# Kernel tuning notes

Hardware: AMD Instinct MI355X
Metric: run time of the kernel (lower is better)

The kernel has to match this reference:

```python
import jax, jax.numpy as jnp
import numpy as np

# dims
B, E, D1, D2 = 16, 384, 64, 64
WS1, WS2 = 8, 8                 # window sizes
H = 12                          # heads
HID = 1536                      # mlp hidden
NW = (D1 // WS1) * (D2 // WS2)  # 64 windows
S = WS1 * WS2                   # 64 tokens per window
DH = E // H                     # 32 head dim


def _layernorm(x, g, b, eps=1e-5):
    mu = jnp.mean(x, axis=-1, keepdims=True)
    var = jnp.var(x, axis=-1, keepdims=True)
    return (x - mu) * jax.lax.rsqrt(var + eps) * g + b


def setup_inputs() -> dict:
    key = jax.random.key(0)
    ks = jax.random.split(key, 10)
    sc = 0.02
    return {
        "x": jax.random.normal(ks[0], (B, E, D1, D2), jnp.float32),
        "mask": jax.random.normal(ks[1], (1, NW, 1, S, S), jnp.float32),
        "ln1_g": jnp.ones((E,), jnp.float32),
        "ln1_b": jnp.zeros((E,), jnp.float32),
        "Wq": sc * jax.random.normal(ks[2], (E, E), jnp.float32),
        "bq": jnp.zeros((E,), jnp.float32),
        "Wk": sc * jax.random.normal(ks[3], (E, E), jnp.float32),
        "bk": jnp.zeros((E,), jnp.float32),
        "Wv": sc * jax.random.normal(ks[4], (E, E), jnp.float32),
        "bv": jnp.zeros((E,), jnp.float32),
        "Wo": sc * jax.random.normal(ks[5], (E, E), jnp.float32),
        "bo": jnp.zeros((E,), jnp.float32),
        "pos_bias": sc * jax.random.normal(ks[6], (1, 1, H, S, S), jnp.float32),
        "ln2_g": jnp.ones((E,), jnp.float32),
        "ln2_b": jnp.zeros((E,), jnp.float32),
        "Wm1": sc * jax.random.normal(ks[7], (E, HID), jnp.float32),
        "bm1": jnp.zeros((HID,), jnp.float32),
        "Wm2": sc * jax.random.normal(ks[8], (HID, E), jnp.float32),
        "bm2": jnp.zeros((E,), jnp.float32),
    }


def reference(x, mask, ln1_g, ln1_b, Wq, bq, Wk, bk, Wv, bv, Wo, bo,
              pos_bias, ln2_g, ln2_b, Wm1, bm1, Wm2, bm2):
    scale = DH ** -0.5
    # channels-last: (b, d1, d2, e)
    xt = jnp.transpose(x, (0, 2, 3, 1))
    xn = _layernorm(xt, ln1_g, ln1_b)
    # cyclic shift (shifted window)
    xn = jnp.roll(xn, (-WS1 // 2, -WS2 // 2), axis=(1, 2))
    # window partition -> (b, nw, s, e)
    xw = xn.reshape(B, D1 // WS1, WS1, D2 // WS2, WS2, E)
    xw = xw.transpose(0, 1, 3, 2, 4, 5).reshape(B, NW, S, E)
    # qkv
    q = (xw @ Wq + bq) * scale
    k = xw @ Wk + bk
    v = xw @ Wv + bv
    q = q.reshape(B, NW, S, H, DH).transpose(0, 1, 3, 2, 4)  # b,w,h,s,d
    k = k.reshape(B, NW, S, H, DH).transpose(0, 1, 3, 2, 4)
    v = v.reshape(B, NW, S, H, DH).transpose(0, 1, 3, 2, 4)
    attn = jnp.einsum('bwhsd,bwhtd->bwhst', q, k) + pos_bias + mask
    attn = jax.nn.softmax(attn, axis=-1)
    z = jnp.einsum('bwhst,bwhtd->bwhsd', attn, v)
    z = z.transpose(0, 1, 3, 2, 4).reshape(B, NW, S, E)
    z = z @ Wo + bo
    # window reverse -> (b, d1, d2, e)
    z = z.reshape(B, D1 // WS1, D2 // WS2, WS1, WS2, E)
    z = z.transpose(0, 1, 3, 2, 4, 5).reshape(B, D1, D2, E)
    z = jnp.roll(z, (WS1 // 2, WS2 // 2), axis=(1, 2))
    xt = xt + z
    # MLP (note: GELU after BOTH linears, faithful to source)
    y = _layernorm(xt, ln2_g, ln2_b)
    y = jax.nn.gelu(y @ Wm1 + bm1, approximate=False)
    y = jax.nn.gelu(y @ Wm2 + bm2, approximate=False)
    xt = xt + y
    # back to channels-first (b, e, d1, d2)
    return jnp.transpose(xt, (0, 3, 1, 2))
```

## Files before the change

kernel.cpp:

```cpp
#include <hip/hip_runtime.h>
#include <hip/hip_bf16.h>
#include <math.h>

#define B_    16
#define E_    384
#define P_    4096
#define NW_   64
#define S_    64
#define H_    12
#define DH_   32
#define HID_  1536
#define T_    65536
#define SHIFT_ 4

typedef unsigned short ushort_t;
typedef __attribute__((ext_vector_type(8))) __bf16 b8;
typedef __attribute__((ext_vector_type(8))) ushort_t u8v;
typedef __attribute__((ext_vector_type(4))) float f4;
typedef __attribute__((ext_vector_type(4))) unsigned u32x4;

__device__ __forceinline__ float u2f(ushort_t u){
    return __uint_as_float(((unsigned)u) << 16);
}
__device__ __forceinline__ ushort_t f2u(float f){
    union { __hip_bfloat16 h; ushort_t u; } cv;
    cv.h = __float2bfloat16(f);
    return cv.u;
}
__device__ __forceinline__ unsigned pack2(float lo, float hi){
    return (unsigned)f2u(lo) | ((unsigned)f2u(hi) << 16);
}
__device__ __forceinline__ float gelu_f(float v){
    const float y2 = v * (1.5957691216057308f + 0.0713548162726f * v * v);
    return v * __builtin_amdgcn_rcpf(1.f + __expf(-y2));
}

#define MFMA(a,b,c) __builtin_amdgcn_mfma_f32_16x16x32_bf16((a),(b),(c),0,0,0)

#define GL2LDS(gp, lp) \
    __builtin_amdgcn_global_load_lds((const __attribute__((address_space(1))) void*)(gp), \
                                     (__attribute__((address_space(3))) void*)(lp), 16, 0, 0)

template<int PERM>
__device__ __forceinline__ int rowmap(int m){
    if (PERM == 0) return m;
    const int bl = m >> 12, wn = (m >> 6) & 63, sd = m & 63;
    const int i_ = ((wn >> 3) << 3) + (sd >> 3);
    const int j_ = ((wn & 7) << 3) + (sd & 7);
    const int d1 = (i_ + SHIFT_) & 63;
    const int d2 = (j_ + SHIFT_) & 63;
    return (bl << 12) + (d1 << 6) + d2;
}

__device__ void wt_body(int bx, int by, int tid,
    const float* __restrict__ src, ushort_t* __restrict__ dst, int K, int N,
    float scale, const float* __restrict__ gv)
{
    __shared__ float t[32][33];
    const int k0 = bx * 32, n0 = by * 32;
    const int c = tid & 31, r = tid >> 5;
    for (int rr = r; rr < 32; rr += 8)
        t[rr][c] = src[(size_t)(k0 + rr) * N + n0 + c];
    __syncthreads();
    const float gg = (gv ? gv[k0 + c] : 1.f) * scale;
    for (int rr = r; rr < 32; rr += 8)
        dst[(size_t)(n0 + rr) * K + k0 + c] = f2u(t[c][rr] * gg);
}

__device__ void lnfold_body(int bx, int tid,
    const float* __restrict__ W, const float* __restrict__ g,
    const float* __restrict__ bt, float scale, int N,
    float* __restrict__ S1, float* __restrict__ S2)
{
    __shared__ float r1[8][32], r2[8][32];
    const int c = tid & 31, ks = tid >> 5;
    const int n = bx * 32 + c;
    float s1 = 0.f, s2 = 0.f;
#pragma unroll
    for (int i = 0; i < 48; ++i){
        const int k = ks * 48 + i;
        const float w = W[(size_t)k * N + n];
        s1 += g[k] * w;
        s2 += bt[k] * w;
    }
    r1[ks][c] = s1; r2[ks][c] = s2;
    __syncthreads();
    if (tid < 32){
        float a = 0.f, b2 = 0.f;
#pragma unroll
        for (int j = 0; j < 8; ++j){ a += r1[j][tid]; b2 += r2[j][tid]; }
        S1[bx * 32 + tid] = a * scale;
        S2[bx * 32 + tid] = b2 * scale;
    }
}

__global__ __launch_bounds__(256) void prep_all(
    const float* Wq, const float* Wk, const float* Wv, const float* Wo,
    const float* Wm1, const float* Wm2,
    const float* ln1_g, const float* ln1_b,
    const float* ln2_g, const float* ln2_b,
    const float* bq, const float* bk, const float* bv,
    ushort_t* Wqkvt, ushort_t* Wot, ushort_t* Wm1t, ushort_t* Wm2t,
    float* S1q, float* S2q, float* S1m, float* S2m, float* bqkv)
{
    const float qscale = 0.17677669529663687f;
    const int id = blockIdx.x, tid = threadIdx.x;
    if (id < 144)       wt_body(id % 12, id / 12, tid, Wq, Wqkvt, E_, E_, qscale, ln1_g);
    else if (id < 288){ const int l = id - 144; wt_body(l % 12, l / 12, tid, Wk, Wqkvt + 384 * E_, E_, E_, 1.f, ln1_g); }
    else if (id < 432){ const int l = id - 288; wt_body(l % 12, l / 12, tid, Wv, Wqkvt + 768 * E_, E_, E_, 1.f, ln1_g); }
    else if (id < 576){ const int l = id - 432; wt_body(l % 12, l / 12, tid, Wo, Wot, E_, E_, 1.f, nullptr); }
    else if (id < 1152){ const int l = id - 576; wt_body(l % 12, l / 12, tid, Wm1, Wm1t, E_, HID_, 1.f, ln2_g); }
    else if (id < 1728){ const int l = id - 1152; wt_body(l % 48, l / 48, tid, Wm2, Wm2t, HID_, E_, 1.f, nullptr); }
    else if (id < 1740) lnfold_body(id - 1728, tid, Wq, ln1_g, ln1_b, qscale, E_, S1q, S2q);
    else if (id < 1752) lnfold_body(id - 1740, tid, Wk, ln1_g, ln1_b, 1.f, E_, S1q + 384, S2q + 384);
    else if (id < 1764) lnfold_body(id - 1752, tid, Wv, ln1_g, ln1_b, 1.f, E_, S1q + 768, S2q + 768);
    else if (id < 1812) lnfold_body(id - 1764, tid, Wm1, ln2_g, ln2_b, 1.f, HID_, S1m, S2m);
    else {
        const int i = (id - 1812) * 256 + tid;
        if (i < 1152){
            float v;
            if (i < 384)      v = bq[i] * qscale;
            else if (i < 768) v = bk[i - 384];
            else              v = bv[i - 768];
            bqkv[i] = v;
        }
    }
}

__global__ __launch_bounds__(256) void k1_ln_window(
    const float* __restrict__ x, ushort_t* __restrict__ xt,
    float* __restrict__ mu1w, float* __restrict__ rs1w)
{
    __shared__ ushort_t tile[64][E_ + 2];
    __shared__ float redS[4][64], redQ[4][64];
    const int b = blockIdx.y, p0 = blockIdx.x * 64, tid = threadIdx.x;

    {
        const int pq = tid & 15, e00 = tid >> 4;
        const float* xp = x + ((size_t)b * E_ + e00) * P_ + p0 + pq * 4;
        f4 v[24];
#pragma unroll
        for (int i = 0; i < 24; ++i)
            v[i] = *(const f4*)(xp + (size_t)(i * 16) * P_);
        float s0 = 0.f, s1 = 0.f, s2 = 0.f, s3 = 0.f;
        float q0 = 0.f, q1 = 0.f, q2 = 0.f, q3 = 0.f;
#pragma unroll
        for (int i = 0; i < 24; ++i){
            const int e = e00 + i * 16;
            tile[pq * 4 + 0][e] = f2u(v[i][0]);
            tile[pq * 4 + 1][e] = f2u(v[i][1]);
            tile[pq * 4 + 2][e] = f2u(v[i][2]);
            tile[pq * 4 + 3][e] = f2u(v[i][3]);
            s0 += v[i][0]; q0 += v[i][0] * v[i][0];
            s1 += v[i][1]; q1 += v[i][1] * v[i][1];
            s2 += v[i][2]; q2 += v[i][2] * v[i][2];
            s3 += v[i][3]; q3 += v[i][3] * v[i][3];
        }
        s0 += __shfl_xor(s0, 16); q0 += __shfl_xor(q0, 16);
        s1 += __shfl_xor(s1, 16); q1 += __shfl_xor(q1, 16);
        s2 += __shfl_xor(s2, 16); q2 += __shfl_xor(q2, 16);
        s3 += __shfl_xor(s3, 16); q3 += __shfl_xor(q3, 16);
        s0 += __shfl_xor(s0, 32); q0 += __shfl_xor(q0, 32);
        s1 += __shfl_xor(s1, 32); q1 += __shfl_xor(q1, 32);
        s2 += __shfl_xor(s2, 32); q2 += __shfl_xor(q2, 32);
        s3 += __shfl_xor(s3, 32); q3 += __shfl_xor(q3, 32);
        const int lane = tid & 63, wvi = tid >> 6;
        if (lane < 16){
            redS[wvi][pq * 4 + 0] = s0; redQ[wvi][pq * 4 + 0] = q0;
            redS[wvi][pq * 4 + 1] = s1; redQ[wvi][pq * 4 + 1] = q1;
            redS[wvi][pq * 4 + 2] = s2; redQ[wvi][pq * 4 + 2] = q2;
            redS[wvi][pq * 4 + 3] = s3; redQ[wvi][pq * 4 + 3] = q3;
        }
    }
    __syncthreads();
    if (tid < 64){
        const float s  = redS[0][tid] + redS[1][tid] + redS[2][tid] + redS[3][tid];
        const float ss = redQ[0][tid] + redQ[1][tid] + redQ[2][tid] + redQ[3][tid];
        const float mu = s / E_;
        const float rs = rsqrtf(ss / E_ - mu * mu + 1e-5f);
        const int p = p0 + tid;
        const int d1 = p >> 6, d2 = p & 63;
        const int i_ = (d1 + 64 - SHIFT_) & 63;
        const int j_ = (d2 + 64 - SHIFT_) & 63;
        const int wsd = ((((i_ >> 3) << 3) + (j_ >> 3)) << 6)
                      + ((i_ & 7) << 3) + (j_ & 7);
        mu1w[b * P_ + wsd] = mu;
        rs1w[b * P_ + wsd] = rs;
    }

    unsigned* xtu = (unsigned*)xt;
    for (int it = 0; it < 48; ++it){
        const int idx = it * 256 + tid;
        const int pj = idx / 192, ep = idx - pj * 192;
        xtu[((size_t)b * P_ + p0 + pj) * 192 + ep] = *(const unsigned*)&tile[pj][ep * 2];
    }
}

template<int KST, int AS, int OS, int MODE, int LNF, int PERM>
__global__ __launch_bounds__(256, 3) void gemm128(
    const ushort_t* __restrict__ A, const ushort_t* __restrict__ Bm,
    const float* __restrict__ bias, ushort_t* __restrict__ out,
    const float* __restrict__ mu, const float* __restrict__ rs,
    const float* __restrict__ S1, const float* __restrict__ S2,
    const ushort_t* __restrict__ resid)
{
    __shared__ __align__(16) ushort_t lds[24576];
    const int tid = threadIdx.x, lane = tid & 63, wv = tid >> 6;
    const int l15 = lane & 15, l4 = lane >> 4;
    const int wr = wv >> 1, wc = wv & 1;

    const int gx = gridDim.x;
    const int nwg = gx * gridDim.y;
    const int d = blockIdx.y * gx + blockIdx.x;
    const int cpx = nwg >> 3;
    const int lb = (d & 7) * cpx + (d >> 3);
    const int n0 = (lb % gx) * 128;
    const size_t m0 = (size_t)(lb / gx) * 128;

    const int kq = tid & 3;
    const int xq = kq ^ ((tid >> 3) & 3);
    size_t aoff0, aoff1, boff0, boff1;
    {
        const int r0 = (int)m0 + (tid >> 2);
        aoff0 = (size_t)rowmap<PERM>(r0) * AS + xq * 8;
        aoff1 = (size_t)rowmap<PERM>(r0 + 64) * AS + xq * 8;
        const int nr = n0 + (tid >> 2);
        boff0 = (size_t)nr * (KST * 32) + xq * 8;
        boff1 = boff0 + (size_t)64 * (KST * 32);
    }

#define STG(cur, k0) do { \
        ushort_t* dst_ = lds + (cur) * 8192; \
        GL2LDS(A + aoff0 + (k0), dst_ + tid * 8); \
        GL2LDS(A + aoff1 + (k0), dst_ + (256 + tid) * 8); \
        GL2LDS(Bm + boff0 + (k0), dst_ + 4096 + tid * 8); \
        GL2LDS(Bm + boff1 + (k0), dst_ + 4096 + (256 + tid) * 8); \
    } while (0)

    f4 acc[4][4];
#pragma unroll
    for (int i = 0; i < 4; ++i)
#pragma unroll
        for (int j = 0; j < 4; ++j) acc[i][j] = (f4){0.f, 0.f, 0.f, 0.f};

    const int rq = (l4 ^ ((l15 >> 1) & 3)) * 8;

    STG(0, 0);
    STG(1, 32);
    for (int ks = 0; ks < KST; ++ks){
        if (ks < KST - 1) asm volatile("s_waitcnt vmcnt(4)" ::: "memory");
        else              asm volatile("s_waitcnt vmcnt(0)" ::: "memory");
        __builtin_amdgcn_s_barrier();
        asm volatile("" ::: "memory");
        if (ks + 2 < KST) STG((ks + 2) % 3, (ks + 2) * 32);
        asm volatile("" ::: "memory");
        const ushort_t* Al = lds + (ks % 3) * 8192;
        const ushort_t* Bl = Al + 4096;
        b8 ax[4], aw[4];
#pragma unroll
        for (int f = 0; f < 4; ++f){
            ax[f] = *(const b8*)(Al + (wr * 64 + f * 16 + l15) * 32 + rq);
            aw[f] = *(const b8*)(Bl + (wc * 64 + f * 16 + l15) * 32 + rq);
        }
        __builtin_amdgcn_s_setprio(1);
#pragma unroll
        for (int fm = 0; fm < 4; ++fm)
#pragma unroll
            for (int fn = 0; fn < 4; ++fn)
                acc[fm][fn] = MFMA(aw[fn], ax[fm], acc[fm][fn]);
        __builtin_amdgcn_s_setprio(0);
    }
#undef STG

    if (MODE == 4){
        float* Tf = (float*)lds;
        float* outf = (float*)out;
#pragma unroll
        for (int rg = 0; rg < 4; ++rg){
            __syncthreads();
            if (wr == (rg >> 1)){
#pragma unroll
                for (int f2h = 0; f2h < 2; ++f2h){
                    const int fm = (rg & 1) * 2 + f2h;
                    const int m5 = f2h * 16 + l15;
                    const int grow = (int)m0 + rg * 32 + m5;
#pragma unroll
                    for (int fn = 0; fn < 4; ++fn){
                        const f4 v = acc[fm][fn];
                        const int nc = wc * 64 + fn * 16 + l4 * 4;
                        const f4 bb = *(const f4*)(bias + n0 + nc);
                        const uint2 ov = *(const uint2*)(resid + (size_t)grow * E_ + n0 + nc);
                        Tf[(nc + 0) * 36 + m5] = u2f((ushort_t)ov.x)         + gelu_f(v[0] + bb[0]);
                        Tf[(nc + 1) * 36 + m5] = u2f((ushort_t)(ov.x >> 16)) + gelu_f(v[1] + bb[1]);
                        Tf[(nc + 2) * 36 + m5] = u2f((ushort_t)ov.y)         + gelu_f(v[2] + bb[2]);
                        Tf[(nc + 3) * 36 + m5] = u2f((ushort_t)(ov.y >> 16)) + gelu_f(v[3] + bb[3]);
                    }
                }
            }
            __syncthreads();
            {
                const int growb = (int)m0 + rg * 32;
                const int bl = growb >> 12, p12 = growb & 4095;
                const int po = (tid & 3) * 4;
#pragma unroll
                for (int eh = 0; eh < 2; ++eh){
                    const int e = eh * 64 + (tid >> 2);
                    float* op = outf + ((size_t)bl * E_ + n0 + e) * P_ + p12 + po;
                    const float* tp = &Tf[e * 36 + po];
                    __builtin_nontemporal_store(*(const f4*)tp, (f4*)op);
                    __builtin_nontemporal_store(*(const f4*)(tp + 16), (f4*)(op + 16));
                }
            }
        }
        return;
    }

    ushort_t* bounce = lds + wv * 2304;
    const int l8r = lane >> 3, l8c = lane & 7;
#pragma unroll
    for (int hh = 0; hh < 2; ++hh){
#pragma unroll
        for (int f2 = 0; f2 < 2; ++f2){
            const int fm = hh * 2 + f2;
            float mur = 0.f, rsr = 1.f;
            if (LNF){
                const int gm = (int)m0 + wr * 64 + fm * 16 + l15;
                mur = mu[gm]; rsr = rs[gm];
            }
#pragma unroll
            for (int fn = 0; fn < 4; ++fn){
                const f4 v = acc[fm][fn];
                const int nc = n0 + wc * 64 + fn * 16 + l4 * 4;
                const f4 bb = *(const f4*)(bias + nc);
                f4 w;
                if (LNF){
                    const f4 s1 = *(const f4*)(S1 + nc);
                    const f4 s2 = *(const f4*)(S2 + nc);
#pragma unroll
                    for (int r = 0; r < 4; ++r)
                        w[r] = rsr * v[r] - rsr * mur * s1[r] + s2[r] + bb[r];
                } else {
#pragma unroll
                    for (int r = 0; r < 4; ++r) w[r] = v[r] + bb[r];
                }
                uint2 pk;
                if (MODE == 1 || MODE == 2){
                    pk.x = pack2(gelu_f(w[0]), gelu_f(w[1]));
                    pk.y = pack2(gelu_f(w[2]), gelu_f(w[3]));
                } else {
                    pk.x = pack2(w[0], w[1]);
                    pk.y = pack2(w[2], w[3]);
                }
                *(uint2*)(bounce + (f2 * 16 + l15) * 72 + fn * 16 + l4 * 4) = pk;
            }
        }
#pragma unroll
        for (int i = 0; i < 4; ++i){
            const int br = i * 8 + l8r;
            const int grow = (int)m0 + wr * 64 + hh * 32 + br;
            const b8 yv = *(const b8*)(bounce + br * 72 + l8c * 8);
            size_t orow;
            if (MODE == 3){
                orow = (size_t)rowmap<1>(grow);
            } else {
                orow = (size_t)grow;
            }
            ushort_t* px = out + orow * OS + n0 + wc * 64 + l8c * 8;
            if (MODE >= 2){
                const b8 ov = *(const b8*)px;
                union { b8 v; unsigned u[4]; } o;
#pragma unroll
                for (int j = 0; j < 4; ++j)
                    o.u[j] = pack2((float)ov[2 * j] + (float)yv[2 * j],
                                   (float)ov[2 * j + 1] + (float)yv[2 * j + 1]);
                *(b8*)px = o.v;
            } else if (MODE == 0){
                union { b8 v; u32x4 q; } t; t.v = yv;
                __builtin_nontemporal_store(t.q, (u32x4*)px);
            } else {
                *(b8*)px = yv;
            }
        }
    }
}

__global__ __launch_bounds__(256) void k2b_attn(
    const ushort_t* __restrict__ qkv,
    const float* __restrict__ pb, const float* __restrict__ mk,
    ushort_t* __restrict__ z)
{
    __shared__ __align__(16) ushort_t q_lds[64 * 32];
    __shared__ __align__(16) ushort_t k_lds[64 * 32];
    __shared__ __align__(16) ushort_t vt_lds[32 * 72];
    __shared__ __align__(16) ushort_t P_lds[64 * 72];

    const int w = blockIdx.x, bl = blockIdx.y, hz = blockIdx.z;
    const int tid = threadIdx.x, lane = tid & 63, wv = tid >> 6;
    const int l15 = lane & 15, l4 = lane >> 4;
    const int rowbase = (bl * NW_ + w) * S_;

    const int srow = tid >> 2, sqp = tid & 3;
    const int sfq = sqp ^ ((srow >> 1) & 3);
    const ushort_t* gql = qkv + (size_t)(rowbase + srow) * 1152 + sfq * 8;
    const ushort_t* gvl = qkv + (size_t)(rowbase + srow) * 1152 + 768 + sqp * 8;

    f4 mkr[4];
#pragma unroll
    for (int nt = 0; nt < 4; ++nt){
        const int t = nt * 16 + l15;
#pragma unroll
        for (int r = 0; r < 4; ++r){
            const int sw = wv * 16 + l4 * 4 + r;
            mkr[nt][r] = mk[((size_t)w * S_ + sw) * S_ + t];
        }
    }

    for (int hi = 0; hi < 4; ++hi){
        const int h = hz * 4 + hi;
        const int hb = h * 32;
        GL2LDS(gql + hb, q_lds + tid * 8);
        GL2LDS(gql + 384 + hb, k_lds + tid * 8);
        {
            const u8v vv = *(const u8v*)(gvl + hb);
#pragma unroll
            for (int j = 0; j < 8; ++j)
                vt_lds[(sqp * 8 + j) * 72 + srow] = vv[j];
        }
        __syncthreads();

        {
            const int qr = wv * 16 + l15;
            const int uq = qr * 4 + (l4 ^ ((qr >> 1) & 3));
            const b8 qfrag = *(const b8*)(&q_lds[uq * 8]);
            f4 sacc[4];
#pragma unroll
            for (int nt = 0; nt < 4; ++nt){
                const int kr = nt * 16 + l15;
                const int uk = kr * 4 + (l4 ^ ((kr >> 1) & 3));
                const b8 kfrag = *(const b8*)(&k_lds[uk * 8]);
                f4 c = (f4){0.f, 0.f, 0.f, 0.f};
                c = MFMA(qfrag, kfrag, c);
                const int t = nt * 16 + l15;
#pragma unroll
                for (int r = 0; r < 4; ++r){
                    const int sw = wv * 16 + l4 * 4 + r;
                    c[r] += pb[((size_t)h * S_ + sw) * S_ + t] + mkr[nt][r];
                }
                sacc[nt] = c;
            }
#pragma unroll
            for (int r = 0; r < 4; ++r){
                float m = fmaxf(fmaxf(sacc[0][r], sacc[1][r]),
                                fmaxf(sacc[2][r], sacc[3][r]));
                m = fmaxf(m, __shfl_xor(m, 1));
                m = fmaxf(m, __shfl_xor(m, 2));
                m = fmaxf(m, __shfl_xor(m, 4));
                m = fmaxf(m, __shfl_xor(m, 8));
                const float e0 = __expf(sacc[0][r] - m), e1 = __expf(sacc[1][r] - m);
                const float e2 = __expf(sacc[2][r] - m), e3 = __expf(sacc[3][r] - m);
                float s = e0 + e1 + e2 + e3;
                s += __shfl_xor(s, 1); s += __shfl_xor(s, 2);
                s += __shfl_xor(s, 4); s += __shfl_xor(s, 8);
                const float inv = __builtin_amdgcn_rcpf(s);
                const int row = wv * 16 + l4 * 4 + r;
                P_lds[row * 72 +      l15] = f2u(e0 * inv);
                P_lds[row * 72 + 16 + l15] = f2u(e1 * inv);
                P_lds[row * 72 + 32 + l15] = f2u(e2 * inv);
                P_lds[row * 72 + 48 + l15] = f2u(e3 * inv);
            }
        }

        {
            f4 zacc[2];
#pragma unroll
            for (int nt = 0; nt < 2; ++nt) zacc[nt] = (f4){0.f, 0.f, 0.f, 0.f};
#pragma unroll
            for (int kb = 0; kb < 2; ++kb){
                const b8 pfrag = *(const b8*)(&P_lds[(wv * 16 + l15) * 72 + kb * 32 + l4 * 8]);
#pragma unroll
                for (int nt = 0; nt < 2; ++nt){
                    const b8 vfrag = *(const b8*)(&vt_lds[(nt * 16 + l15) * 72 + kb * 32 + l4 * 8]);
                    zacc[nt] = MFMA(pfrag, vfrag, zacc[nt]);
                }
            }
#pragma unroll
            for (int nt = 0; nt < 2; ++nt)
#pragma unroll
                for (int r = 0; r < 4; ++r){
                    const int row = wv * 16 + l4 * 4 + r;
                    z[(size_t)(rowbase + row) * E_ + hb + nt * 16 + l15] = f2u(zacc[nt][r]);
                }
        }
        __syncthreads();
    }
}

__global__ __launch_bounds__(256) void ln2_stats(
    const ushort_t* __restrict__ xt, float* __restrict__ mu2, float* __restrict__ rs2)
{
    const int tid = threadIdx.x;
    const int lr = blockIdx.x * 64 + (tid >> 2), q = tid & 3;
    const ushort_t* rp = xt + (size_t)lr * E_;
    float s = 0.f, ss = 0.f;
#pragma unroll
    for (int i = 0; i < 12; ++i){
        const b8 v = *(const b8*)(rp + q * 8 + i * 32);
#pragma unroll
        for (int j = 0; j < 8; ++j){ const float f = (float)v[j]; s += f; ss += f * f; }
    }
    s += __shfl_xor(s, 1); ss += __shfl_xor(ss, 1);
    s += __shfl_xor(s, 2); ss += __shfl_xor(ss, 2);
    if (q == 0){
        const float m = s * (1.f / E_);
        mu2[lr] = m;
        rs2[lr] = rsqrtf(ss * (1.f / E_) - m * m + 1e-5f);
    }
}

__global__ __launch_bounds__(256) void k4_out(
    const ushort_t* __restrict__ xt, float* __restrict__ out)
{
    __shared__ float tile[32][68];
    const int b = blockIdx.z, p0 = blockIdx.x * 64, e0 = blockIdx.y * 32;
    const int tid = threadIdx.x;
    {
        const int r = tid >> 2, c = tid & 3;
        const u8v v = *(const u8v*)(xt + ((size_t)b * P_ + p0 + r) * E_ + e0 + c * 8);
#pragma unroll
        for (int j = 0; j < 8; ++j)
            tile[c * 8 + j][r] = u2f(v[j]);
    }
    __syncthreads();
    {
        const int er = tid >> 3, pc = tid & 7;
        float* op = out + ((size_t)b * E_ + e0 + er) * P_ + p0 + pc * 8;
        const f4 v0 = *(const f4*)&tile[er][pc * 8];
        const f4 v1 = *(const f4*)&tile[er][pc * 8 + 4];
        __builtin_nontemporal_store(v0, (f4*)op);
        __builtin_nontemporal_store(v1, (f4*)(op + 4));
    }
}

extern "C" void kernel_launch(void* const* d_in, const int* in_sizes, int n_in,
                              void* d_out, int out_size, void* d_ws, size_t ws_size,
                              hipStream_t stream)
{
    const float* x      = (const float*)d_in[0];
    const float* mask   = (const float*)d_in[1];
    const float* ln1_g  = (const float*)d_in[2];
    const float* ln1_b  = (const float*)d_in[3];
    const float* Wq     = (const float*)d_in[4];
    const float* bq     = (const float*)d_in[5];
    const float* Wk     = (const float*)d_in[6];
    const float* bk     = (const float*)d_in[7];
    const float* Wv     = (const float*)d_in[8];
    const float* bv     = (const float*)d_in[9];
    const float* Wo     = (const float*)d_in[10];
    const float* bo     = (const float*)d_in[11];
    const float* pos_b  = (const float*)d_in[12];
    const float* ln2_g  = (const float*)d_in[13];
    const float* ln2_b  = (const float*)d_in[14];
    const float* Wm1    = (const float*)d_in[15];
    const float* bm1    = (const float*)d_in[16];
    const float* Wm2    = (const float*)d_in[17];
    const float* bm2    = (const float*)d_in[18];

    ushort_t* xt = (ushort_t*)d_ws;
    const bool bigws = ws_size >= (size_t)103022592;
    ushort_t* scratch = (ushort_t*)d_out;

    if (bigws){
        ushort_t* qkvb  = scratch;
        ushort_t* Wqkvt = scratch + 37748736;
        ushort_t* Wot   = Wqkvt + 1152 * E_;
        float*    bqkv  = (float*)(scratch + 38338560);
        float*    S1q   = (float*)(scratch + 38340864);
        float*    S2q   = (float*)(scratch + 38343168);
        float*    S1m   = (float*)(scratch + 38345472);
        float*    S2m   = (float*)(scratch + 38348544);
        float*    mu1w  = (float*)(scratch + 38351616);
        float*    rs1w  = (float*)(scratch + 38482688);
        float*    mu2   = (float*)(scratch + 38613760);
        float*    rs2   = (float*)(scratch + 38744832);
        ushort_t* zb    = xt + 25165824;
        ushort_t* hbuf  = xt + 25165824;
        ushort_t* Wm1t  = xt + 50331648;
        ushort_t* Wm2t  = Wm1t + E_ * HID_;

        prep_all<<<1817, 256, 0, stream>>>(Wq, Wk, Wv, Wo, Wm1, Wm2,
            ln1_g, ln1_b, ln2_g, ln2_b, bq, bk, bv,
            Wqkvt, Wot, Wm1t, Wm2t, S1q, S2q, S1m, S2m, bqkv);

        k1_ln_window<<<dim3(P_ / 64, B_), 256, 0, stream>>>(x, xt, mu1w, rs1w);

        for (int mc = 0; mc < 2; ++mc){
            ushort_t* xtc = xt + (size_t)mc * 32768 * E_;
            gemm128<12, E_, 1152, 0, 1, 1><<<dim3(9, 256), 256, 0, stream>>>(
                xtc, Wqkvt, bqkv, qkvb, mu1w + (size_t)mc * 32768,
                rs1w + (size_t)mc * 32768, S1q, S2q, nullptr);
            k2b_attn<<<dim3(NW_, 8, 3), 256, 0, stream>>>(qkvb, pos_b, mask, zb);
            gemm128<12, E_, E_, 3, 0, 0><<<dim3(3, 256), 256, 0, stream>>>(
                zb, Wot, bo, xtc, nullptr, nullptr, nullptr, nullptr, nullptr);
        }

        ln2_stats<<<T_ / 64, 256, 0, stream>>>(xt, mu2, rs2);
        for (int mc = 0; mc < 4; ++mc){
            ushort_t* xtc = xt + (size_t)mc * 16384 * E_;
            gemm128<12, E_, HID_, 1, 1, 0><<<dim3(HID_ / 128, 128), 256, 0, stream>>>(
                xtc, Wm1t, bm1, hbuf, mu2 + (size_t)mc * 16384,
                rs2 + (size_t)mc * 16384, S1m, S2m, nullptr);
            ushort_t* outc = (ushort_t*)((float*)d_out + (size_t)(mc * 4) * E_ * P_);
            gemm128<48, HID_, E_, 4, 0, 0><<<dim3(E_ / 128, 128), 256, 0, stream>>>(
                hbuf, Wm2t, bm2, outc, nullptr, nullptr, nullptr, nullptr, xtc);
        }
    } else {
        ushort_t* zb    = scratch;
        ushort_t* hbuf  = scratch;
        ushort_t* Wqkvt = scratch + 25165824;
        ushort_t* Wot   = Wqkvt + 1152 * E_;
        ushort_t* Wm1t  = Wot + E_ * E_;
        ushort_t* Wm2t  = Wm1t + E_ * HID_;
        ushort_t* qkvb  = scratch + 26935296;
        float*    bqkv  = (float*)(scratch + 45809664);
        float*    S1q   = (float*)(scratch + 45811968);
        float*    S2q   = (float*)(scratch + 45814272);
        float*    S1m   = (float*)(scratch + 45816576);
        float*    S2m   = (float*)(scratch + 45819648);
        float*    mu1w  = (float*)(scratch + 45822720);
        float*    rs1w  = (float*)(scratch + 45953792);
        float*    mu2   = (float*)(scratch + 46084864);
        float*    rs2   = (float*)(scratch + 46215936);

        prep_all<<<1817, 256, 0, stream>>>(Wq, Wk, Wv, Wo, Wm1, Wm2,
            ln1_g, ln1_b, ln2_g, ln2_b, bq, bk, bv,
            Wqkvt, Wot, Wm1t, Wm2t, S1q, S2q, S1m, S2m, bqkv);

        k1_ln_window<<<dim3(P_ / 64, B_), 256, 0, stream>>>(x, xt, mu1w, rs1w);

        for (int mc = 0; mc < 4; ++mc){
            ushort_t* xtc = xt + (size_t)mc * 16384 * E_;
            gemm128<12, E_, 1152, 0, 1, 1><<<dim3(9, 128), 256, 0, stream>>>(
                xtc, Wqkvt, bqkv, qkvb, mu1w + (size_t)mc * 16384,
                rs1w + (size_t)mc * 16384, S1q, S2q, nullptr);
            k2b_attn<<<dim3(NW_, 4, 3), 256, 0, stream>>>(qkvb, pos_b, mask, zb);
            gemm128<12, E_, E_, 3, 0, 0><<<dim3(3, 128), 256, 0, stream>>>(
                zb, Wot, bo, xtc, nullptr, nullptr, nullptr, nullptr, nullptr);
        }

        ln2_stats<<<T_ / 64, 256, 0, stream>>>(xt, mu2, rs2);
        for (int mc = 0; mc < 4; ++mc){
            ushort_t* xtc = xt + (size_t)mc * 16384 * E_;
            gemm128<12, E_, HID_, 1, 1, 0><<<dim3(HID_ / 128, 128), 256, 0, stream>>>(
                xtc, Wm1t, bm1, hbuf, mu2 + (size_t)mc * 16384,
                rs2 + (size_t)mc * 16384, S1m, S2m, nullptr);
            gemm128<48, HID_, E_, 2, 0, 0><<<dim3(E_ / 128, 128), 256, 0, stream>>>(
                hbuf, Wm2t, bm2, xtc, nullptr, nullptr, nullptr, nullptr, nullptr);
        }
        k4_out<<<dim3(P_ / 64, E_ / 32, B_), 256, 0, stream>>>(xt, (float*)d_out);
    }
}
```

Measured before the change: 519.9 us.

## Fuse LN2 statistics into Wo GEMM epilogue via atomic row sums

The Wo projection epilogue, which already adds the residual, now also accumulates per-row sum and sum-of-squares of the updated residual through shuffle reductions and float atomics. The MLP1 GEMM derives mean and rsqrt-variance from these sums, so the separate ln2_stats pass that re-read the whole residual tensor is dropped. The accumulators are zeroed in the prep kernel. This trades one full read of the activation for atomic traffic in the epilogue and a less numerically stable variance formula (E[x^2]-mean^2), computed on values before bf16 rounding.

Result: no change. 528.1 us (+1.6%).

```diff
diff --git a/kernel.cpp b/kernel.cpp
--- a/kernel.cpp
+++ b/kernel.cpp
@@ -101,7 +101,8 @@
     const float* ln2_g, const float* ln2_b,
     const float* bq, const float* bk, const float* bv,
     ushort_t* Wqkvt, ushort_t* Wot, ushort_t* Wm1t, ushort_t* Wm2t,
-    float* S1q, float* S2q, float* S1m, float* S2m, float* bqkv)
+    float* S1q, float* S2q, float* S1m, float* S2m, float* bqkv,
+    float* zacc)
 {
     const float qscale = 0.17677669529663687f;
     const int id = blockIdx.x, tid = threadIdx.x;
@@ -115,7 +116,7 @@
     else if (id < 1752) lnfold_body(id - 1740, tid, Wk, ln1_g, ln1_b, 1.f, E_, S1q + 384, S2q + 384);
     else if (id < 1764) lnfold_body(id - 1752, tid, Wv, ln1_g, ln1_b, 1.f, E_, S1q + 768, S2q + 768);
     else if (id < 1812) lnfold_body(id - 1764, tid, Wm1, ln2_g, ln2_b, 1.f, HID_, S1m, S2m);
-    else {
+    else if (id < 1817){
         const int i = (id - 1812) * 256 + tid;
         if (i < 1152){
             float v;
@@ -124,6 +125,9 @@
             else              v = bv[i - 768];
             bqkv[i] = v;
         }
+    } else {
+        const int zi = (id - 1817) * 256 + tid;
+        if (zi < 2 * T_) zacc[zi] = 0.f;
     }
 }
 
@@ -202,7 +206,8 @@
     const float* __restrict__ bias, ushort_t* __restrict__ out,
     const float* __restrict__ mu, const float* __restrict__ rs,
     const float* __restrict__ S1, const float* __restrict__ S2,
-    const ushort_t* __restrict__ resid)
+    const ushort_t* __restrict__ resid,
+    float* __restrict__ sA, float* __restrict__ ssA)
 {
     __shared__ __align__(16) ushort_t lds[24576];
     const int tid = threadIdx.x, lane = tid & 63, wv = tid >> 6;
@@ -323,9 +328,14 @@
         for (int f2 = 0; f2 < 2; ++f2){
             const int fm = hh * 2 + f2;
             float mur = 0.f, rsr = 1.f;
-            if (LNF){
+            if (LNF == 1){
                 const int gm = (int)m0 + wr * 64 + fm * 16 + l15;
                 mur = mu[gm]; rsr = rs[gm];
+            } else if (LNF == 2){
+                const int gm = (int)m0 + wr * 64 + fm * 16 + l15;
+                const float sv = mu[gm], ssv = rs[gm];
+                mur = sv * (1.f / E_);
+                rsr = rsqrtf(ssv * (1.f / E_) - mur * mur + 1e-5f);
             }
 #pragma unroll
             for (int fn = 0; fn < 4; ++fn){
@@ -369,11 +379,24 @@
             if (MODE >= 2){
                 const b8 ov = *(const b8*)px;
                 union { b8 v; unsigned u[4]; } o;
-#pragma unroll
-                for (int j = 0; j < 4; ++j)
-                    o.u[j] = pack2((float)ov[2 * j] + (float)yv[2 * j],
-                                   (float)ov[2 * j + 1] + (float)yv[2 * j + 1]);
+                float sp = 0.f, qp = 0.f;
+#pragma unroll
+                for (int j = 0; j < 4; ++j){
+                    const float t0 = (float)ov[2 * j]     + (float)yv[2 * j];
+                    const float t1 = (float)ov[2 * j + 1] + (float)yv[2 * j + 1];
+                    o.u[j] = pack2(t0, t1);
+                    if (MODE == 3){ sp += t0 + t1; qp += t0 * t0 + t1 * t1; }
+                }
                 *(b8*)px = o.v;
+                if (MODE == 3){
+                    sp += __shfl_xor(sp, 1); qp += __shfl_xor(qp, 1);
+                    sp += __shfl_xor(sp, 2); qp += __shfl_xor(qp, 2);
+                    sp += __shfl_xor(sp, 4); qp += __shfl_xor(qp, 4);
+                    if (l8c == 0){
+                        atomicAdd(sA + orow, sp);
+                        atomicAdd(ssA + orow, qp);
+                    }
+                }
             } else if (MODE == 0){
                 union { b8 v; u32x4 q; } t; t.v = yv;
                 __builtin_nontemporal_store(t.q, (u32x4*)px);
@@ -580,16 +603,16 @@
         float*    S2m   = (float*)(scratch + 38348544);
         float*    mu1w  = (float*)(scratch + 38351616);
         float*    rs1w  = (float*)(scratch + 38482688);
-        float*    mu2   = (float*)(scratch + 38613760);
-        float*    rs2   = (float*)(scratch + 38744832);
+        float*    sA    = (float*)(scratch + 38613760);
+        float*    ssA   = (float*)(scratch + 38744832);
         ushort_t* zb    = xt + 25165824;
         ushort_t* hbuf  = xt + 25165824;
         ushort_t* Wm1t  = xt + 50331648;
         ushort_t* Wm2t  = Wm1t + E_ * HID_;
 
-        prep_all<<<1817, 256, 0, stream>>>(Wq, Wk, Wv, Wo, Wm1, Wm2,
+        prep_all<<<2329, 256, 0, stream>>>(Wq, Wk, Wv, Wo, Wm1, Wm2,
             ln1_g, ln1_b, ln2_g, ln2_b, bq, bk, bv,
-            Wqkvt, Wot, Wm1t, Wm2t, S1q, S2q, S1m, S2m, bqkv);
+            Wqkvt, Wot, Wm1t, Wm2t, S1q, S2q, S1m, S2m, bqkv, sA);
 
         k1_ln_window<<<dim3(P_ / 64, B_), 256, 0, stream>>>(x, xt, mu1w, rs1w);
 
@@ -597,21 +620,22 @@
             ushort_t* xtc = xt + (size_t)mc * 32768 * E_;
             gemm128<12, E_, 1152, 0, 1, 1><<<dim3(9, 256), 256, 0, stream>>>(
                 xtc, Wqkvt, bqkv, qkvb, mu1w + (size_t)mc * 32768,
-                rs1w + (size_t)mc * 32768, S1q, S2q, nullptr);
+                rs1w + (size_t)mc * 32768, S1q, S2q, nullptr, nullptr, nullptr);
             k2b_attn<<<dim3(NW_, 8, 3), 256, 0, stream>>>(qkvb, pos_b, mask, zb);
             gemm128<12, E_, E_, 3, 0, 0><<<dim3(3, 256), 256, 0, stream>>>(
-                zb, Wot, bo, xtc, nullptr, nullptr, nullptr, nullptr, nullptr);
-        }
-
-        ln2_stats<<<T_ / 64, 256, 0, stream>>>(xt, mu2, rs2);
+                zb, Wot, bo, xtc, nullptr, nullptr, nullptr, nullptr, nullptr,
+                sA + (size_t)mc * 32768, ssA + (size_t)mc * 32768);
+        }
+
         for (int mc = 0; mc < 4; ++mc){
             ushort_t* xtc = xt + (size_t)mc * 16384 * E_;
-            gemm128<12, E_, HID_, 1, 1, 0><<<dim3(HID_ / 128, 128), 256, 0, stream>>>(
-                xtc, Wm1t, bm1, hbuf, mu2 + (size_t)mc * 16384,
-                rs2 + (size_t)mc * 16384, S1m, S2m, nullptr);
+            gemm128<12, E_, HID_, 1, 2, 0><<<dim3(HID_ / 128, 128), 256, 0, stream>>>(
+                xtc, Wm1t, bm1, hbuf, sA + (size_t)mc * 16384,
+                ssA + (size_t)mc * 16384, S1m, S2m, nullptr, nullptr, nullptr);
             ushort_t* outc = (ushort_t*)((float*)d_out + (size_t)(mc * 4) * E_ * P_);
             gemm128<48, HID_, E_, 4, 0, 0><<<dim3(E_ / 128, 128), 256, 0, stream>>>(
-                hbuf, Wm2t, bm2, outc, nullptr, nullptr, nullptr, nullptr, xtc);
+                hbuf, Wm2t, bm2, outc, nullptr, nullptr, nullptr, nullptr, xtc,
+                nullptr, nullptr);
         }
     } else {
         ushort_t* zb    = scratch;
@@ -631,9 +655,9 @@
         float*    mu2   = (float*)(scratch + 46084864);
         float*    rs2   = (float*)(scratch + 46215936);
 
-        prep_all<<<1817, 256, 0, stream>>>(Wq, Wk, Wv, Wo, Wm1, Wm2,
+        prep_all<<<2329, 256, 0, stream>>>(Wq, Wk, Wv, Wo, Wm1, Wm2,
             ln1_g, ln1_b, ln2_g, ln2_b, bq, bk, bv,
-            Wqkvt, Wot, Wm1t, Wm2t, S1q, S2q, S1m, S2m, bqkv);
+            Wqkvt, Wot, Wm1t, Wm2t, S1q, S2q, S1m, S2m, bqkv, mu2);
 
         k1_ln_window<<<dim3(P_ / 64, B_), 256, 0, stream>>>(x, xt, mu1w, rs1w);
 
@@ -641,10 +665,11 @@
             ushort_t* xtc = xt + (size_t)mc * 16384 * E_;
             gemm128<12, E_, 1152, 0, 1, 1><<<dim3(9, 128), 256, 0, stream>>>(
                 xtc, Wqkvt, bqkv, qkvb, mu1w + (size_t)mc * 16384,
-                rs1w + (size_t)mc * 16384, S1q, S2q, nullptr);
+                rs1w + (size_t)mc * 16384, S1q, S2q, nullptr, nullptr, nullptr);
             k2b_attn<<<dim3(NW_, 4, 3), 256, 0, stream>>>(qkvb, pos_b, mask, zb);
-            gemm128<12, E_, E_, 3, 0, 0><<<dim3(3, 128), 256, 0, stream>>>(
-                zb, Wot, bo, xtc, nullptr, nullptr, nullptr, nullptr, nullptr);
+            gemm128<12, E_, E_, 2, 0, 0><<<dim3(3, 128), 256, 0, stream>>>(
+                zb, Wot, bo, xtc, nullptr, nullptr, nullptr, nullptr, nullptr,
+                nullptr, nullptr);
         }
 
         ln2_stats<<<T_ / 64, 256, 0, stream>>>(xt, mu2, rs2);
@@ -652,9 +677,10 @@
             ushort_t* xtc = xt + (size_t)mc * 16384 * E_;
             gemm128<12, E_, HID_, 1, 1, 0><<<dim3(HID_ / 128, 128), 256, 0, stream>>>(
                 xtc, Wm1t, bm1, hbuf, mu2 + (size_t)mc * 16384,
-                rs2 + (size_t)mc * 16384, S1m, S2m, nullptr);
+                rs2 + (size_t)mc * 16384, S1m, S2m, nullptr, nullptr, nullptr);
             gemm128<48, HID_, E_, 2, 0, 0><<<dim3(E_ / 128, 128), 256, 0, stream>>>(
-                hbuf, Wm2t, bm2, xtc, nullptr, nullptr, nullptr, nullptr, nullptr);
+                hbuf, Wm2t, bm2, xtc, nullptr, nullptr, nullptr, nullptr, nullptr,
+                nullptr, nullptr);
         }
         k4_out<<<dim3(P_ / 64, E_ / 32, B_), 256, 0, stream>>>(xt, (float*)d_out);
     }
```
